# Kernel tuning notes

Hardware: AMD Instinct MI355X
Metric: run time of the kernel (lower is better)

## Reference

```python
import jax, jax.numpy as jnp
import numpy as np

B, L, DIM, HEADS = 4, 1024, 512, 8
HD = DIM // HEADS
HID = max(64, DIM // 2)
WIN = 32
SPARSITY = 0.3
TEMP = 1.0
PAT_TAU = 0.5


def setup_inputs() -> dict:
    key = jax.random.key(0)
    ks = jax.random.split(key, 8)
    gn = lambda k, shape, sc: jax.random.normal(k, shape, jnp.float32) * sc
    return {
        "x": jax.random.normal(ks[0], (B, L, DIM), jnp.float32),
        "mask": jnp.ones((B, L), jnp.int32),
        "Wqkv": gn(ks[1], (3 * DIM, DIM), 0.02),
        "Wproj": gn(ks[2], (DIM, DIM), 0.02),
        "bproj": jnp.zeros((DIM,), jnp.float32),
        "Wsel1": gn(ks[3], (HID, DIM), 0.05),
        "bsel1": jnp.zeros((HID,), jnp.float32),
        "Wsel2": gn(ks[4], (3, HID), 0.05),
        "bsel2": jnp.zeros((3,), jnp.float32),
        "log_pattern_tau": jnp.asarray(np.log(PAT_TAU), jnp.float32),
        "sparse_w": gn(ks[5], (HEADS,), 0.2),
        "sparse_b": jnp.zeros((HEADS,), jnp.float32),
    }


def reference(x, mask, Wqkv, Wproj, bproj, Wsel1, bsel1, Wsel2, bsel2,
              log_pattern_tau, sparse_w, sparse_b):
    Bq, Lq, D = x.shape
    scale = HD ** -0.5
    qkv = (x @ Wqkv.T).reshape(Bq, Lq, 3, HEADS, HD)
    q = jnp.transpose(qkv[:, :, 0], (0, 2, 1, 3))  # (B,H,L,hd)
    k = jnp.transpose(qkv[:, :, 1], (0, 2, 1, 3))
    v = jnp.transpose(qkv[:, :, 2], (0, 2, 1, 3))
    scores = jnp.einsum('bhid,bhjd->bhij', q, k) * scale  # (B,H,L,L)

    # pattern selector on mean-pooled features (eval: no gumbel, no dropout)
    pooled = x.mean(axis=1)
    logits = jax.nn.relu(pooled @ Wsel1.T + bsel1) @ Wsel2.T + bsel2  # (B,3)
    tau = jnp.clip(jnp.exp(log_pattern_tau), 1e-4, 10.0)
    pw = jax.nn.softmax(logits / tau, axis=-1)  # (B,3)

    half = WIN // 2
    ii = jnp.arange(Lq)[:, None]
    jj = jnp.arange(Lq)[None, :]
    local = ((jj >= ii - half) & (jj <= ii + half)).astype(jnp.float32)

    # learned sparse top-k mask per head via kth-value threshold
    kk = max(1, int(Lq * (1.0 - SPARSITY)))
    s = scores * sparse_w[None, :, None, None] + sparse_b[None, :, None, None]
    kth = jax.lax.top_k(s, kk)[0][..., -1:]
    smask = (s >= kth).astype(jnp.float32)  # (B,H,L,L)

    combined = (pw[:, 0, None, None, None] * local[None, None]
                + pw[:, 1, None, None, None]
                + pw[:, 2, None, None, None] * smask)
    neg = jnp.float32(-1e9)
    scores = jnp.where(combined > 0.05, scores, neg)
    scores = jnp.where(mask[:, None, None, :] == 0, neg, scores)

    # fallback: if a row is fully masked, unmask position 0
    all_masked = jnp.all(scores <= neg + 1e-6, axis=-1)  # (B,H,L)
    scores = scores.at[..., 0].set(jnp.where(all_masked, 0.0, scores[..., 0]))

    attn = jax.nn.softmax(scores / TEMP, axis=-1)
    out = jnp.einsum('bhij,bhjd->bhid', attn, v)
    out = jnp.transpose(out, (0, 2, 1, 3)).reshape(Bq, Lq, D)
    return out @ Wproj.T + bproj
```

## Files before the change

### kernel.cpp

```cpp
#include <hip/hip_runtime.h>
#include <math.h>

typedef __attribute__((ext_vector_type(8))) short short8;
typedef __attribute__((ext_vector_type(4))) float floatx4;

#define MFMA16(a, b, c) __builtin_amdgcn_mfma_f32_16x16x32_bf16(a, b, c, 0, 0, 0)

extern "C" __device__ float __ocml_native_exp2_f32(float);


#define FRAG512(row, k) (((size_t)((row) >> 4)) * 8192 + (((k) >> 5) * 512) + \
                         ((((k) >> 3) & 3) * 128) + (((row) & 15) * 8) + ((k) & 7))
#define FRAGQK(row, e)  (((size_t)((row) >> 4)) * 1024 + (((e) >> 5) * 512) + \
                         ((((e) >> 3) & 3) * 128) + (((row) & 15) * 8) + ((e) & 7))

#define OFF_XB    ((size_t)0)
#define OFF_WQKV  ((size_t)4194304)
#define OFF_WPROJ ((size_t)5767168)
#define OFF_Q     ((size_t)6291456)
#define OFF_K     ((size_t)10485760)
#define OFF_VT    ((size_t)14680064)
#define OFF_AT    ((size_t)18874368)
#define OFF_PW    ((size_t)23068672)
#define OFF_PAR   ((size_t)23069696)
#define OFF_W1T   ((size_t)23595008)

__device__ __forceinline__ unsigned short f2bf(float f) {
    unsigned u = __float_as_uint(f);
    return (unsigned short)((u + 0x7fffu + ((u >> 16) & 1u)) >> 16);
}
__device__ __forceinline__ float bf2f(unsigned short s) {
    return __uint_as_float((unsigned)s << 16);
}
__device__ __forceinline__ unsigned cvt_pk_bf16(float lo, float hi) {
    unsigned r;
    asm("v_cvt_pk_bf16_f32 %0, %1, %2" : "=v"(r) : "v"(lo), "v"(hi));
    return r;
}
__device__ __forceinline__ void gl16(const void* g, void* l) {
    __builtin_amdgcn_global_load_lds(
        (const __attribute__((address_space(1))) unsigned*)g,
        (__attribute__((address_space(3))) unsigned*)l, 16, 0, 0);
}

__device__ __forceinline__ void frag_cvt_tile(const float* __restrict__ src,
                                              unsigned short* __restrict__ dst,
                                              const int t, const float sc)
{
    const int ln = t & 15, quad = (t >> 4) & 3, kh = t >> 6;
    #pragma unroll
    for (int i = 0; i < 4; ++i) {
        const int kb = kh + i * 4;
        const float* s = src + (size_t)ln * 512 + kb * 32 + quad * 8;
        float4 f0 = *(const float4*)s;
        float4 f1 = *(const float4*)(s + 4);
        unsigned o01 = cvt_pk_bf16(f0.x * sc, f0.y * sc);
        unsigned o23 = cvt_pk_bf16(f0.z * sc, f0.w * sc);
        unsigned o45 = cvt_pk_bf16(f1.x * sc, f1.y * sc);
        unsigned o67 = cvt_pk_bf16(f1.z * sc, f1.w * sc);
        unsigned short* d = dst + kb * 512 + (size_t)(t & 63) * 8;
        *(uint2*)d       = make_uint2(o01, o23);
        *(uint2*)(d + 4) = make_uint2(o45, o67);
    }
}

__global__ __launch_bounds__(256)
void cvt_all(const float* __restrict__ x, const float* __restrict__ wqkv,
             const float* __restrict__ wproj, const float* __restrict__ W1,
             unsigned short* __restrict__ xb, unsigned short* __restrict__ oq,
             unsigned short* __restrict__ op, float* __restrict__ partial,
             float* __restrict__ w1t)
{
    const int bid = blockIdx.x, t = threadIdx.x;
    if (bid < 256) {
        const int rt = bid;
        const float* src = x + (size_t)rt * 16 * 512;
        frag_cvt_tile(src, xb + (size_t)rt * 8192, t, 1.f);
        float s0 = 0.f, s1 = 0.f;
        #pragma unroll 4
        for (int l = 0; l < 16; ++l) {
            s0 += src[(size_t)l * 512 + t];
            s1 += src[(size_t)l * 512 + t + 256];
        }
        partial[(size_t)rt * 512 + t] = s0;
        partial[(size_t)rt * 512 + t + 256] = s1;
    } else if (bid < 384) {
        const int tile = bid - 256;
        if (tile < 96)
            frag_cvt_tile(wqkv + (size_t)tile * 16 * 512, oq + (size_t)tile * 8192, t, 1.f);
        else
            frag_cvt_tile(wproj + (size_t)(tile - 96) * 16 * 512,
                          op + (size_t)(tile - 96) * 8192, t, 1.f);
    } else {
        __shared__ float tl[64][65];
        const int tile = bid - 384;
        const int tr = tile >> 3, tc = tile & 7;
        const int lr = t >> 6, lc = t & 63;
        #pragma unroll
        for (int p = 0; p < 16; ++p) {
            const int r = p * 4 + lr;
            tl[r][lc] = W1[(size_t)(tr * 64 + r) * 512 + tc * 64 + lc];
        }
        __syncthreads();
        #pragma unroll
        for (int p = 0; p < 16; ++p) {
            const int d = p * 4 + lr;
            w1t[(size_t)(tc * 64 + d) * 256 + tr * 64 + lc] = tl[lc][d];
        }
    }
}

__global__ __launch_bounds__(256)
void gemm_qkv_sel(const unsigned short* __restrict__ xb, const unsigned short* __restrict__ wb,
                  unsigned short* __restrict__ qo, unsigned short* __restrict__ ko,
                  unsigned short* __restrict__ vo,
                  const float* __restrict__ partial, const float* __restrict__ w1t,
                  const float* __restrict__ b1, const float* __restrict__ W2,
                  const float* __restrict__ b2, const float* __restrict__ ltau,
                  float* __restrict__ pwout)
{
    __shared__ __align__(16) unsigned short tile[4][64 * 72];
    const int t = threadIdx.x;
    const int w = t >> 6, l64 = t & 63;

    if (blockIdx.y == 32) {
        if (blockIdx.x >= 4) return;
        const int b = blockIdx.x;
        float* pooled = (float*)&tile[0][0];
        float* hpart  = pooled + 512;
        float* h1s    = hpart + 1024;
        float* lg     = h1s + 256;
        #pragma unroll
        for (int c = 0; c < 2; ++c) {
            const int col = t + c * 256;
            float s = 0.f;
            for (int p = 0; p < 64; ++p) s += partial[((size_t)b * 64 + p) * 512 + col];
            pooled[col] = s * (1.f / 1024.f);
        }
        __syncthreads();
        {
            float4 acc = make_float4(0.f, 0.f, 0.f, 0.f);
            const float* wt = w1t + (size_t)w * 128 * 256 + l64 * 4;
            for (int d = 0; d < 128; ++d) {
                const float pv = pooled[w * 128 + d];
                float4 wv = *(const float4*)(wt + (size_t)d * 256);
                acc.x += pv * wv.x; acc.y += pv * wv.y;
                acc.z += pv * wv.z; acc.w += pv * wv.w;
            }
            *(float4*)&hpart[w * 256 + l64 * 4] = acc;
        }
        __syncthreads();
        h1s[t] = fmaxf(hpart[t] + hpart[256 + t] + hpart[512 + t] + hpart[768 + t] + b1[t], 0.f);
        __syncthreads();
        if (t < 3) {
            float s = b2[t];
            const float* w2 = W2 + t * 256;
            for (int i = 0; i < 256; ++i) s += w2[i] * h1s[i];
            float tauv = fminf(fmaxf(expf(ltau[0]), 1e-4f), 10.f);
            lg[t] = s / tauv;
        }
        __syncthreads();
        if (t == 0) {
            float m = fmaxf(lg[0], fmaxf(lg[1], lg[2]));
            float e0 = expf(lg[0] - m), e1 = expf(lg[1] - m), e2 = expf(lg[2] - m);
            float inv = 1.f / (e0 + e1 + e2);
            pwout[b * 3 + 0] = e0 * inv;
            pwout[b * 3 + 1] = e1 * inv;
            pwout[b * 3 + 2] = e2 * inv;
        }
        return;
    }

    const int wg = blockIdx.y * 12 + blockIdx.x;
    const int sw_id = (wg & 7) * 48 + (wg >> 3);
    const int bx = sw_id % 12, by = sw_id / 12;

    const int ln = l64 & 15, quad = l64 >> 4;
    const int m0  = (by << 7) + ((w >> 1) << 6);
    const int nb0 = (bx << 7) + ((w & 1) << 6);

    const unsigned short* Abase = xb + ((size_t)(m0 >> 4)) * 8192 + l64 * 8;
    const unsigned short* Bbase = wb + ((size_t)(nb0 >> 4)) * 8192 + l64 * 8;

    floatx4 acc[4][4];
    #pragma unroll
    for (int i = 0; i < 4; ++i)
        #pragma unroll
        for (int j = 0; j < 4; ++j) acc[i][j] = (floatx4){0.f, 0.f, 0.f, 0.f};

    short8 a0[4], b0[4], a1[4], b1v[4];
    #pragma unroll
    for (int i = 0; i < 4; ++i) {
        a0[i] = *(const short8*)(Abase + (size_t)i * 8192);
        b0[i] = *(const short8*)(Bbase + (size_t)i * 8192);
    }
    for (int s = 0; s < 16; s += 2) {
        #pragma unroll
        for (int i = 0; i < 4; ++i) {
            a1[i]  = *(const short8*)(Abase + (size_t)i * 8192 + (s + 1) * 512);
            b1v[i] = *(const short8*)(Bbase + (size_t)i * 8192 + (s + 1) * 512);
        }
        #pragma unroll
        for (int i = 0; i < 4; ++i)
            #pragma unroll
            for (int j = 0; j < 4; ++j)
                acc[i][j] = MFMA16(a0[i], b0[j], acc[i][j]);
        if (s + 2 < 16) {
            #pragma unroll
            for (int i = 0; i < 4; ++i) {
                a0[i] = *(const short8*)(Abase + (size_t)i * 8192 + (s + 2) * 512);
                b0[i] = *(const short8*)(Bbase + (size_t)i * 8192 + (s + 2) * 512);
            }
        }
        #pragma unroll
        for (int i = 0; i < 4; ++i)
            #pragma unroll
            for (int j = 0; j < 4; ++j)
                acc[i][j] = MFMA16(a1[i], b1v[j], acc[i][j]);
    }

    unsigned short* tw = &tile[w][0];
    const int which = nb0 >> 9;
    const int hh = (nb0 >> 6) & 7;
    const int g = (m0 >> 10) * 8 + hh;
    const int lrow0 = m0 & 1023;

    if (which == 2) {
        #pragma unroll
        for (int j = 0; j < 4; ++j)
            #pragma unroll
            for (int i = 0; i < 4; ++i) {
                unsigned u01 = cvt_pk_bf16(acc[i][j][0], acc[i][j][1]);
                unsigned u23 = cvt_pk_bf16(acc[i][j][2], acc[i][j][3]);
                *(uint2*)&tw[(j * 16 + ln) * 72 + i * 16 + quad * 4] = make_uint2(u01, u23);
            }
        const int chunk = lrow0 >> 7;
        const int ks0 = (lrow0 & 127) >> 5;
        unsigned short* dst = vo + (size_t)g * 65536 + (size_t)chunk * 8192;
        #pragma unroll
        for (int et = 0; et < 4; ++et)
            #pragma unroll
            for (int ksl = 0; ksl < 2; ++ksl) {
                const unsigned short* srcp = &tw[(et * 16 + ln) * 72 + ksl * 32 + quad * 8];
                *(short8*)(dst + (et * 4 + ks0 + ksl) * 512 + l64 * 8) = *(const short8*)srcp;
            }
    } else {
        const float sc = (which == 0) ? 0.180336880f : 1.f;
        #pragma unroll
        for (int j = 0; j < 4; ++j)
            #pragma unroll
            for (int i = 0; i < 4; ++i) {
                unsigned u01 = cvt_pk_bf16(acc[i][j][0] * sc, acc[i][j][1] * sc);
                unsigned u23 = cvt_pk_bf16(acc[i][j][2] * sc, acc[i][j][3] * sc);
                const int rb = (i * 16 + quad * 4) * 72 + j * 16 + ln;
                tw[rb]           = (unsigned short)u01;
                tw[rb + 72]      = (unsigned short)(u01 >> 16);
                tw[rb + 144]     = (unsigned short)u23;
                tw[rb + 216]     = (unsigned short)(u23 >> 16);
            }
        unsigned short* dst = (which == 0 ? qo : ko) + (size_t)g * 65536;
        #pragma unroll
        for (int rt = 0; rt < 4; ++rt)
            #pragma unroll
            for (int eh = 0; eh < 2; ++eh) {
                const unsigned short* srcp = &tw[(rt * 16 + ln) * 72 + eh * 32 + quad * 8];
                *(short8*)(dst + ((size_t)((lrow0 >> 4) + rt)) * 1024 + eh * 512 + l64 * 8) =
                    *(const short8*)srcp;
            }
    }
}

__global__ __launch_bounds__(256)
void gemm_proj(const unsigned short* __restrict__ ab, const unsigned short* __restrict__ wb,
               const float* __restrict__ bias, float* __restrict__ out)
{
    const int t = threadIdx.x;
    const int w = t >> 6, l64 = t & 63;
    const int ln = l64 & 15, quad = l64 >> 4;

    const int wg = blockIdx.y * 4 + blockIdx.x;
    const int sw_id = (wg & 7) * 32 + (wg >> 3);
    const int n0 = ((sw_id & 3) << 7) + ((w & 1) << 6);
    const int m0 = ((sw_id >> 2) << 6) + ((w >> 1) << 5);

    const unsigned short* Abase = ab + ((size_t)(m0 >> 4)) * 8192 + l64 * 8;
    const unsigned short* Bbase = wb + ((size_t)(n0 >> 4)) * 8192 + l64 * 8;

    floatx4 acc[2][4];
    #pragma unroll
    for (int i = 0; i < 2; ++i)
        #pragma unroll
        for (int j = 0; j < 4; ++j) acc[i][j] = (floatx4){0.f, 0.f, 0.f, 0.f};

    short8 a0[2], b0[4], a1[2], b1v[4];
    #pragma unroll
    for (int i = 0; i < 2; ++i) a0[i] = *(const short8*)(Abase + (size_t)i * 8192);
    #pragma unroll
    for (int j = 0; j < 4; ++j) b0[j] = *(const short8*)(Bbase + (size_t)j * 8192);
    for (int s = 0; s < 16; s += 2) {
        #pragma unroll
        for (int i = 0; i < 2; ++i) a1[i]  = *(const short8*)(Abase + (size_t)i * 8192 + (s + 1) * 512);
        #pragma unroll
        for (int j = 0; j < 4; ++j) b1v[j] = *(const short8*)(Bbase + (size_t)j * 8192 + (s + 1) * 512);
        #pragma unroll
        for (int i = 0; i < 2; ++i)
            #pragma unroll
            for (int j = 0; j < 4; ++j)
                acc[i][j] = MFMA16(a0[i], b0[j], acc[i][j]);
        if (s + 2 < 16) {
            #pragma unroll
            for (int i = 0; i < 2; ++i) a0[i] = *(const short8*)(Abase + (size_t)i * 8192 + (s + 2) * 512);
            #pragma unroll
            for (int j = 0; j < 4; ++j) b0[j] = *(const short8*)(Bbase + (size_t)j * 8192 + (s + 2) * 512);
        }
        #pragma unroll
        for (int i = 0; i < 2; ++i)
            #pragma unroll
            for (int j = 0; j < 4; ++j)
                acc[i][j] = MFMA16(a1[i], b1v[j], acc[i][j]);
    }
    #pragma unroll
    for (int j = 0; j < 4; ++j) {
        const float bv = bias[n0 + j * 16 + ln];
        #pragma unroll
        for (int i = 0; i < 2; ++i)
            #pragma unroll
            for (int reg = 0; reg < 4; ++reg)
                out[(size_t)(m0 + i * 16 + quad * 4 + reg) * 512 + n0 + j * 16 + ln] =
                    acc[i][j][reg] + bv;
    }
}

__global__ __launch_bounds__(256)
void attn_flash(const unsigned short* __restrict__ qm, const unsigned short* __restrict__ km,
                const unsigned short* __restrict__ vm, const int* __restrict__ mask,
                const float* __restrict__ pw, const float* __restrict__ sw,
                const float* __restrict__ sb, unsigned short* __restrict__ aout)
{
    __shared__ int mk[1024];
    __shared__ __align__(16) unsigned short Ks[2][8192];
    __shared__ __align__(16) unsigned short Vs[8192];
    __shared__ __align__(16) unsigned short Pws[4][2176];
    __shared__ unsigned kths[4][16];

    const int t = threadIdx.x;
    const int w = t >> 6, l64 = t & 63;
    const int ln = l64 & 15, quad = l64 >> 4;
    const int g = blockIdx.x & 31;
    const int rg = blockIdx.x >> 5;
    const int b = g >> 3, h = g & 7;
    const int i0 = rg * 64 + w * 16;

    const unsigned short* qg = qm + (size_t)g * 65536;
    const unsigned short* kg = km + (size_t)g * 65536;
    const unsigned short* vg = vm + (size_t)g * 65536;

    *(int4*)&mk[t * 4] = *(const int4*)(mask + b * 1024 + t * 4);

    const float pw0 = pw[b * 3 + 0], pw1 = pw[b * 3 + 1], pw2 = pw[b * 3 + 2];
    const bool a00 = pw1 > 0.05f;
    const bool a10 = (pw0 * 1.0f + pw1) > 0.05f;
    const bool a01 = (pw1 + pw2) > 0.05f;
    const bool a11 = ((pw0 * 1.0f + pw1) + pw2) > 0.05f;
    const bool need_sparse = (!a00 && a01) || (!a10 && a11);
    const bool flat_ok = (!need_sparse) && a00 && a10;
    const float w_h = sw[h], b_h = sb[h];

    #pragma unroll
    for (int c = 0; c < 4; ++c) {
        const int bi = w * 4 + c;
        gl16(kg + bi * 512 + l64 * 8, (char*)Ks[0] + bi * 1024);
    }

    unsigned kth_r[4] = {0u, 0u, 0u, 0u};
    if (need_sparse) {
        unsigned* ub = (unsigned*)((char*)Ks + 16384 + w * 4096);
        for (int r = 0; r < 16; ++r) {
            for (int c = 0; c < 16; ++c) {
                const int col = c * 64 + l64;
                float s = 0.f;
                for (int e = 0; e < 64; ++e)
                    s += bf2f(qg[FRAGQK(i0 + r, e)]) * bf2f(kg[FRAGQK(col, e)]);
                unsigned uu = __float_as_uint(s * w_h + b_h);
                ub[col] = (uu & 0x80000000u) ? ~uu : (uu | 0x80000000u);
            }
            unsigned u[16];
            #pragma unroll
            for (int c = 0; c < 16; ++c) u[c] = ub[l64 + c * 64];
            unsigned act = 0xFFFFu, p = 0u;
            int kk = 716;
            for (int bit = 31; bit >= 0; --bit) {
                unsigned ones = 0u;
                #pragma unroll
                for (int c = 0; c < 16; ++c)
                    if (((act >> c) & 1u) && ((u[c] >> bit) & 1u)) ones |= (1u << c);
                int c1 = __popc(ones);
                for (int off = 32; off; off >>= 1) c1 += __shfl_xor(c1, off);
                if (kk <= c1) { p |= (1u << bit); act &= ones; }
                else          { kk -= c1; act &= ~ones; }
            }
            if (l64 == 0) kths[w][r] = p;
        }
        #pragma unroll
        for (int reg = 0; reg < 4; ++reg) kth_r[reg] = kths[w][quad * 4 + reg];
    }

    const short8 aq0 = *(const short8*)(qg + ((size_t)(i0 >> 4)) * 1024 + l64 * 8);
    const short8 aq1 = *(const short8*)(qg + ((size_t)(i0 >> 4)) * 1024 + 512 + l64 * 8);

    __syncthreads();

    float l_acc[4] = {0.f, 0.f, 0.f, 0.f};
    floatx4 accv[4];
    #pragma unroll
    for (int et = 0; et < 4; ++et) accv[et] = (floatx4){0.f, 0.f, 0.f, 0.f};
    unsigned short* Pw = &Pws[w][0];

    for (int jc = 0; jc < 8; ++jc) {
        const int j0 = jc << 7;
        const int cur = jc & 1;
        const unsigned short* Kc = &Ks[cur][0];
        {
            const unsigned short* vc = vg + (size_t)jc * 8192;
            #pragma unroll
            for (int c = 0; c < 4; ++c) {
                const int bi = w * 4 + c;
                gl16(vc + bi * 512 + l64 * 8, (char*)Vs + bi * 1024);
            }
            if (jc < 7) {
                const unsigned short* kc = kg + (size_t)(jc + 1) * 8192;
                #pragma unroll
                for (int c = 0; c < 4; ++c) {
                    const int bi = w * 4 + c;
                    gl16(kc + bi * 512 + l64 * 8, (char*)Ks[cur ^ 1] + bi * 1024);
                }
            }
        }
        const bool mall = __all((mk[j0 + l64] != 0) && (mk[j0 + 64 + l64] != 0));
        const bool fast = flat_ok && mall;

        floatx4 sfr[8];
        __builtin_amdgcn_s_setprio(1);
        #pragma unroll
        for (int nt = 0; nt < 8; ++nt) {
            const short8 kb0 = *(const short8*)(Kc + nt * 1024 + l64 * 8);
            const short8 kb1 = *(const short8*)(Kc + nt * 1024 + 512 + l64 * 8);
            floatx4 z = (floatx4){0.f, 0.f, 0.f, 0.f};
            z = MFMA16(aq0, kb0, z);
            z = MFMA16(aq1, kb1, z);
            sfr[nt] = z;
        }
        __builtin_amdgcn_s_setprio(0);

        if (!fast) {
            #pragma unroll
            for (int nt = 0; nt < 8; ++nt) {
                const int j = j0 + nt * 16 + ln;
                const bool mk0 = (mk[j] == 0);
                #pragma unroll
                for (int reg = 0; reg < 4; ++reg) {
                    const int i = i0 + quad * 4 + reg;
                    const float s = sfr[nt][reg];
                    const bool loc = (j >= i - 16) && (j <= i + 16);
                    bool sm = false;
                    if (need_sparse) {
                        unsigned uu = __float_as_uint(s * w_h + b_h);
                        unsigned key = (uu & 0x80000000u) ? ~uu : (uu | 0x80000000u);
                        sm = key >= kth_r[reg];
                    }
                    bool allowed = loc ? (sm ? a11 : a10) : (sm ? a01 : a00);
                    if (mk0) allowed = false;
                    sfr[nt][reg] = allowed ? s : -1e9f;
                }
            }
        }
        #pragma unroll
        for (int nt = 0; nt < 8; ++nt) {
            const float p0 = __ocml_native_exp2_f32(sfr[nt][0]);
            const float p1 = __ocml_native_exp2_f32(sfr[nt][1]);
            const float p2 = __ocml_native_exp2_f32(sfr[nt][2]);
            const float p3 = __ocml_native_exp2_f32(sfr[nt][3]);
            l_acc[0] += p0; l_acc[1] += p1; l_acc[2] += p2; l_acc[3] += p3;
            const unsigned u01 = cvt_pk_bf16(p0, p1);
            const unsigned u23 = cvt_pk_bf16(p2, p3);
            const int col = nt * 16 + ln;
            Pw[(quad * 4 + 0) * 136 + col] = (unsigned short)u01;
            Pw[(quad * 4 + 1) * 136 + col] = (unsigned short)(u01 >> 16);
            Pw[(quad * 4 + 2) * 136 + col] = (unsigned short)u23;
            Pw[(quad * 4 + 3) * 136 + col] = (unsigned short)(u23 >> 16);
        }
        short8 pa[4];
        #pragma unroll
        for (int ks = 0; ks < 4; ++ks)
            pa[ks] = *(const short8*)&Pw[ln * 136 + ks * 32 + quad * 8];
        __syncthreads();
        __builtin_amdgcn_s_setprio(1);
        #pragma unroll
        for (int et = 0; et < 4; ++et) {
            floatx4 a = accv[et];
            #pragma unroll
            for (int ks = 0; ks < 4; ++ks) {
                const short8 bv = *(const short8*)(Vs + (et * 4 + ks) * 512 + l64 * 8);
                a = MFMA16(pa[ks], bv, a);
            }
            accv[et] = a;
        }
        __builtin_amdgcn_s_setprio(0);
        __syncthreads();
    }

    #pragma unroll
    for (int reg = 0; reg < 4; ++reg) {
        float v = l_acc[reg];
        v += __shfl_xor(v, 1);
        v += __shfl_xor(v, 2);
        v += __shfl_xor(v, 4);
        v += __shfl_xor(v, 8);
        l_acc[reg] = v;
    }

    float* PO_w = (float*)((char*)Ks + w * 4352);
    #pragma unroll
    for (int et = 0; et < 4; ++et)
        #pragma unroll
        for (int reg = 0; reg < 4; ++reg) {
            float val;
            if (l_acc[reg] == 0.f)
                val = bf2f(vg[et * 2048 + ln * 8]);
            else
                val = accv[et][reg] / l_acc[reg];
            PO_w[(quad * 4 + reg) * 68 + et * 16 + ln] = val;
        }
    #pragma unroll
    for (int rr = 0; rr < 4; ++rr) {
        const int r = (l64 >> 4) * 4 + rr;
        const int cb = (l64 & 15) * 4;
        float4 ov = *(const float4*)&PO_w[r * 68 + cb];
        const unsigned uxy = cvt_pk_bf16(ov.x, ov.y);
        const unsigned uzw = cvt_pk_bf16(ov.z, ov.w);
        const int row_g = b * 1024 + i0 + r;
        const int col = h * 64 + cb;
        *(uint2*)&aout[FRAG512(row_g, col)] = make_uint2(uxy, uzw);
    }
}

extern "C" void kernel_launch(void* const* d_in, const int* in_sizes, int n_in,
                              void* d_out, int out_size, void* d_ws, size_t ws_size,
                              hipStream_t stream) {
    const float* x     = (const float*)d_in[0];
    const int*   mask  = (const int*)d_in[1];
    const float* Wqkv  = (const float*)d_in[2];
    const float* Wproj = (const float*)d_in[3];
    const float* bproj = (const float*)d_in[4];
    const float* Wsel1 = (const float*)d_in[5];
    const float* bsel1 = (const float*)d_in[6];
    const float* Wsel2 = (const float*)d_in[7];
    const float* bsel2 = (const float*)d_in[8];
    const float* ltau  = (const float*)d_in[9];
    const float* sw    = (const float*)d_in[10];
    const float* sb    = (const float*)d_in[11];
    char* ws = (char*)d_ws;
    unsigned short* xb     = (unsigned short*)(ws + OFF_XB);
    unsigned short* wqkvb  = (unsigned short*)(ws + OFF_WQKV);
    unsigned short* wprojb = (unsigned short*)(ws + OFF_WPROJ);
    unsigned short* q      = (unsigned short*)(ws + OFF_Q);
    unsigned short* k      = (unsigned short*)(ws + OFF_K);
    unsigned short* v      = (unsigned short*)(ws + OFF_VT);
    unsigned short* attnb  = (unsigned short*)(ws + OFF_AT);
    float* pw  = (float*)(ws + OFF_PW);
    float* par = (float*)(ws + OFF_PAR);
    float* w1t = (float*)(ws + OFF_W1T);
    float* out = (float*)d_out;
    (void)in_sizes; (void)n_in; (void)out_size; (void)ws_size;

    cvt_all<<<416, 256, 0, stream>>>(x, Wqkv, Wproj, Wsel1, xb, wqkvb, wprojb, par, w1t);
    gemm_qkv_sel<<<dim3(12, 33), 256, 0, stream>>>(xb, wqkvb, q, k, v,
                                                   par, w1t, bsel1, Wsel2, bsel2, ltau, pw);
    attn_flash<<<512, 256, 0, stream>>>(q, k, v, mask, pw, sw, sb, attnb);
    gemm_proj<<<dim3(4, 64), 256, 0, stream>>>(attnb, wprojb, bproj, out);
}
```

Before: 133.9 us.

## Stage QKV GEMM operand tiles through double-buffered LDS via direct global-to-LDS loads

The QKV projection GEMM previously had each wave load its own A and B fragments straight from global memory into registers, so waves sharing a block row or column fetched the same data twice. Now the block cooperatively copies the 128-row A and B slices for each k-step into a double-buffered shared-memory stage using gl16 (global-to-LDS) loads, and each wave reads its fragments from LDS. This halves global traffic per block, at the cost of an extra LDS hop and a block-wide barrier on every k-step. The shared buffer is now a union so the epilogue tile reuses the same memory.

```diff
diff --git a/kernel.cpp b/kernel.cpp
--- a/kernel.cpp
+++ b/kernel.cpp
@@ -119,14 +119,17 @@
                   const float* __restrict__ b2, const float* __restrict__ ltau,
                   float* __restrict__ pwout)
 {
-    __shared__ __align__(16) unsigned short tile[4][64 * 72];
+    __shared__ __align__(16) union SmT {
+        unsigned short stage[2][8192];
+        unsigned short tile[4][4608];
+    } sm;
     const int t = threadIdx.x;
     const int w = t >> 6, l64 = t & 63;
 
     if (blockIdx.y == 32) {
         if (blockIdx.x >= 4) return;
         const int b = blockIdx.x;
-        float* pooled = (float*)&tile[0][0];
+        float* pooled = (float*)&sm.tile[0][0];
         float* hpart  = pooled + 512;
         float* h1s    = hpart + 1024;
         float* lg     = h1s + 256;
@@ -176,11 +179,12 @@
     const int bx = sw_id % 12, by = sw_id / 12;
 
     const int ln = l64 & 15, quad = l64 >> 4;
-    const int m0  = (by << 7) + ((w >> 1) << 6);
-    const int nb0 = (bx << 7) + ((w & 1) << 6);
-
-    const unsigned short* Abase = xb + ((size_t)(m0 >> 4)) * 8192 + l64 * 8;
-    const unsigned short* Bbase = wb + ((size_t)(nb0 >> 4)) * 8192 + l64 * 8;
+    const int mq = w >> 1, nq = w & 1;
+    const int m0  = (by << 7) + (mq << 6);
+    const int nb0 = (bx << 7) + (nq << 6);
+
+    const unsigned short* Ag = xb + ((size_t)(by << 3)) * 8192;
+    const unsigned short* Bg = wb + ((size_t)(bx << 3)) * 8192;
 
     floatx4 acc[4][4];
     #pragma unroll
@@ -188,38 +192,47 @@
         #pragma unroll
         for (int j = 0; j < 4; ++j) acc[i][j] = (floatx4){0.f, 0.f, 0.f, 0.f};
 
-    short8 a0[4], b0[4], a1[4], b1v[4];
-    #pragma unroll
-    for (int i = 0; i < 4; ++i) {
-        a0[i] = *(const short8*)(Abase + (size_t)i * 8192);
-        b0[i] = *(const short8*)(Bbase + (size_t)i * 8192);
-    }
-    for (int s = 0; s < 16; s += 2) {
+    {
+        #pragma unroll
+        for (int c = 0; c < 4; ++c) {
+            const int seg = w * 4 + c;
+            const unsigned short* src = (seg < 8)
+                ? Ag + (size_t)seg * 8192 + l64 * 8
+                : Bg + (size_t)(seg - 8) * 8192 + l64 * 8;
+            gl16(src, (char*)sm.stage[0] + seg * 1024);
+        }
+    }
+    __syncthreads();
+
+    for (int s = 0; s < 16; ++s) {
+        const int cur = s & 1;
+        if (s < 15) {
+            #pragma unroll
+            for (int c = 0; c < 4; ++c) {
+                const int seg = w * 4 + c;
+                const unsigned short* src = (seg < 8)
+                    ? Ag + (size_t)seg * 8192 + (s + 1) * 512 + l64 * 8
+                    : Bg + (size_t)(seg - 8) * 8192 + (s + 1) * 512 + l64 * 8;
+                gl16(src, (char*)sm.stage[cur ^ 1] + seg * 1024);
+            }
+        }
+        const unsigned short* As = sm.stage[cur] + (mq * 4) * 512 + l64 * 8;
+        const unsigned short* Bs = sm.stage[cur] + 4096 + (nq * 4) * 512 + l64 * 8;
+        short8 av[4], bv[4];
         #pragma unroll
         for (int i = 0; i < 4; ++i) {
-            a1[i]  = *(const short8*)(Abase + (size_t)i * 8192 + (s + 1) * 512);
-            b1v[i] = *(const short8*)(Bbase + (size_t)i * 8192 + (s + 1) * 512);
+            av[i] = *(const short8*)(As + i * 512);
+            bv[i] = *(const short8*)(Bs + i * 512);
         }
         #pragma unroll
         for (int i = 0; i < 4; ++i)
             #pragma unroll
             for (int j = 0; j < 4; ++j)
-                acc[i][j] = MFMA16(a0[i], b0[j], acc[i][j]);
-        if (s + 2 < 16) {
-            #pragma unroll
-            for (int i = 0; i < 4; ++i) {
-                a0[i] = *(const short8*)(Abase + (size_t)i * 8192 + (s + 2) * 512);
-                b0[i] = *(const short8*)(Bbase + (size_t)i * 8192 + (s + 2) * 512);
-            }
-        }
-        #pragma unroll
-        for (int i = 0; i < 4; ++i)
-            #pragma unroll
-            for (int j = 0; j < 4; ++j)
-                acc[i][j] = MFMA16(a1[i], b1v[j], acc[i][j]);
-    }
-
-    unsigned short* tw = &tile[w][0];
+                acc[i][j] = MFMA16(av[i], bv[j], acc[i][j]);
+        __syncthreads();
+    }
+
+    unsigned short* tw = &sm.tile[w][0];
     const int which = nb0 >> 9;
     const int hh = (nb0 >> 6) & 7;
     const int g = (m0 >> 10) * 8 + hh;
```

Result: no change. 135.5 us (+1.2%).
